# Kernel tuning notes

Hardware: AMD Instinct MI355X
Metric: run time of the kernel (lower is better)

The kernel has to match this reference:

```python
import jax, jax.numpy as jnp
import numpy as np

B, S, D, H = 2, 2048, 1024, 16
DK = D // H


def setup_inputs() -> dict:
    key = jax.random.key(0)
    ks = jax.random.split(key, 7)
    q = jax.random.normal(ks[0], (B, S, D), dtype=jnp.float32)
    k = jax.random.normal(ks[1], (B, S, D), dtype=jnp.float32)
    v = jax.random.normal(ks[2], (B, S, D), dtype=jnp.float32)
    # causal mask: mask==0 positions get -1e9 before softmax
    mask = jnp.tril(jnp.ones((S, S), dtype=jnp.int32))[None, None, :, :]
    scale = 0.02
    w_q = jax.random.normal(ks[3], (D, D), dtype=jnp.float32) * scale
    w_k = jax.random.normal(ks[4], (D, D), dtype=jnp.float32) * scale
    w_v = jax.random.normal(ks[5], (D, D), dtype=jnp.float32) * scale
    w_o = jax.random.normal(ks[6], (D, D), dtype=jnp.float32) * scale
    return {"q": q, "k": k, "v": v, "mask": mask,
            "w_q": w_q, "w_k": w_k, "w_v": w_v, "w_o": w_o}


def reference(q, k, v, mask, w_q, w_k, w_v, w_o):
    # nn.Linear(bias=False): x @ W.T
    query = q @ w_q.T  # [B,S,D]
    key = k @ w_k.T
    value = v @ w_v.T
    # split heads -> [B,H,S,DK]
    query = query.reshape(B, S, H, DK).transpose(0, 2, 1, 3)
    key = key.reshape(B, S, H, DK).transpose(0, 2, 1, 3)
    value = value.reshape(B, S, H, DK).transpose(0, 2, 1, 3)
    scores = jnp.einsum('bhqd,bhkd->bhqk', query, key) / jnp.sqrt(
        jnp.asarray(DK, dtype=query.dtype))
    scores = jnp.where(mask == 0, jnp.asarray(-1e9, scores.dtype), scores)
    attn = jax.nn.softmax(scores, axis=-1)  # dropout p=0.0 -> identity
    x = jnp.einsum('bhqk,bhkd->bhqd', attn, value)  # [B,H,S,DK]
    x = x.transpose(0, 2, 1, 3).reshape(B, S, D)
    return x @ w_o.T
```

## Files before the change

kernel.cpp:

```cpp
#include <hip/hip_runtime.h>

typedef __attribute__((ext_vector_type(8))) short short8;
typedef __attribute__((ext_vector_type(4))) float f32x4;

#define DEVI static __device__ __forceinline__

constexpr int BB = 2, SS = 2048, DD = 1024, HH = 16, DKK = 64;
constexpr size_t QN = (size_t)BB * SS * DD;
constexpr size_t WN = (size_t)DD * DD;

constexpr size_t OFF_WQ = 3 * QN;
constexpr size_t OFF_WO = OFF_WQ + 3 * WN;
constexpr size_t OFF_QM = OFF_WQ + 4 * WN;
constexpr size_t OFF_KM = OFF_QM + QN;
constexpr size_t OFF_VM = OFF_QM + 2 * QN;
constexpr size_t OFF_XC = OFF_QM + 3 * QN;

DEVI unsigned short f2bf(float f) {
  unsigned int u = __float_as_uint(f);
  u = (u + 0x7fffu + ((u >> 16) & 1u)) >> 16;
  return (unsigned short)u;
}

DEVI f32x4 fzero() { f32x4 z = {0.f, 0.f, 0.f, 0.f}; return z; }

DEVI void gld16(const void* g, void* l) {
  __builtin_amdgcn_global_load_lds((__attribute__((address_space(1))) void*)g,
                                   (__attribute__((address_space(3))) void*)l,
                                   16, 0, 0);
}

DEVI short8 mk8u(unsigned int a, unsigned int b, unsigned int c, unsigned int d) {
  union { short8 s; unsigned int u[4]; } x;
  x.u[0] = a; x.u[1] = b; x.u[2] = c; x.u[3] = d;
  return x.s;
}

DEVI short8 mk8q(unsigned long long lo, unsigned long long hi) {
  union { short8 s; unsigned long long q[2]; } x;
  x.q[0] = lo; x.q[1] = hi;
  return x.s;
}

DEVI unsigned int pkbf(float a, float b) {
  return __builtin_amdgcn_perm(__float_as_uint(b), __float_as_uint(a), 0x07060302u);
}

#define VMBAR(N) asm volatile("s_waitcnt vmcnt(" #N ")\n\ts_barrier" ::: "memory")
#define LGKM0                                      \
  do {                                             \
    asm volatile("s_waitcnt lgkmcnt(0)" ::: "memory"); \
    __builtin_amdgcn_sched_barrier(0);             \
  } while (0)

__global__ __launch_bounds__(256) void convert_all(
    const float* __restrict__ q, const float* __restrict__ k,
    const float* __restrict__ v, const float* __restrict__ wq,
    const float* __restrict__ wk, const float* __restrict__ wv,
    const float* __restrict__ wo, unsigned short* __restrict__ ws) {
  size_t t = (size_t)blockIdx.x * 256 + threadIdx.x;
  size_t e = t * 4;
  const float* src;
  size_t base, idx;
  if (e < 3 * QN) {
    size_t a = e >> 22;
    idx = e & (QN - 1);
    src = (a == 0) ? q : (a == 1) ? k : v;
    base = a * QN;
  } else {
    size_t r = e - 3 * QN;
    size_t a = r >> 20;
    idx = r & (WN - 1);
    src = (a == 0) ? wq : (a == 1) ? wk : (a == 2) ? wv : wo;
    base = 3 * QN + a * WN;
  }
  float4 f = *(const float4*)(src + idx);
  ushort4 o;
  o.x = f2bf(f.x); o.y = f2bf(f.y); o.z = f2bf(f.z); o.w = f2bf(f.w);
  *(ushort4*)(ws + base + idx) = o;
}

__global__ __launch_bounds__(512, 2) void proj_gemm(unsigned short* __restrict__ ws) {
  __shared__ unsigned short lds[65536];
  const int tid = threadIdx.x;
  const int w = tid >> 6, l = tid & 63;
  const int lr = l & 15, qd = l >> 4, l7 = l & 7, l3 = l >> 3;
  const int wr = w >> 2, wc = w & 3;

  const int orig = blockIdx.x;
  const int swz = (orig & 7) * 24 + (orig >> 3);
  const int mt = swz >> 2, nt = swz & 3;
  const int z = mt >> 4;
  const int m0 = (mt & 15) * 256, n0 = nt * 256;

  const unsigned short* Ab = ws + (size_t)z * QN;
  const unsigned short* Wb = ws + OFF_WQ + (size_t)z * WN;
  unsigned short* O = ws + OFF_QM + (size_t)z * QN;

  const bool vz = (z == 2);
  const unsigned short* src0 = vz ? Ab : Wb;
  const unsigned short* src1 = vz ? Wb : Ab;
  const int base0 = vz ? m0 : n0;
  const int base1 = vz ? n0 : m0;

  f32x4 acc[8][4];
#pragma unroll
  for (int i = 0; i < 8; ++i)
#pragma unroll
    for (int j = 0; j < 4; ++j) acc[i][j] = fzero();

  auto stage = [&](int buf, int ab, int h, int kt) {
    const unsigned short* src = ab ? src1 : src0;
    const int rc0 = (ab ? base1 : base0) + h * 128 + w * 8 + l3;
    const int kofs = kt * 64 + ((l7 ^ l3) * 8);
    unsigned short* d = &lds[buf * 32768 + ab * 16384 + h * 8192 + w * 512];
#pragma unroll
    for (int u = 0; u < 2; ++u)
      gld16(src + (size_t)(rc0 + u * 64) * DD + kofs, d + u * 4096);
  };
  auto rdA = [&](int buf, int fi, int ks) -> short8 {
    const int rg = (fi * 2 + wr) * 16 + lr;
    const int c2 = (ks * 4 + qd) ^ l7;
    return *(const short8*)&lds[buf * 32768 + rg * 64 + c2 * 8];
  };
  auto rdB = [&](int buf, int fj, int ks) -> short8 {
    const int rg = (fj * 4 + wc) * 16 + lr;
    const int c2 = (ks * 4 + qd) ^ l7;
    return *(const short8*)&lds[buf * 32768 + 16384 + rg * 64 + c2 * 8];
  };

  stage(0, 0, 0, 0);
  stage(0, 1, 0, 0);
  stage(0, 1, 1, 0);
  stage(0, 0, 1, 0);

  constexpr int NT = DD / 64;
#pragma unroll 1
  for (int t = 0; t < NT; ++t) {
    const int rb = t & 1, wb = rb ^ 1;
    const bool g = (t + 1 < NT);
    short8 af[4][2], bf[2][2], bh[2][2];

    VMBAR(4);
    if (g) stage(wb, 0, 0, t + 1);
#pragma unroll
    for (int mi = 0; mi < 4; ++mi)
#pragma unroll
      for (int ks = 0; ks < 2; ++ks) af[mi][ks] = rdA(rb, mi, ks);
#pragma unroll
    for (int nj = 0; nj < 2; ++nj)
#pragma unroll
      for (int ks = 0; ks < 2; ++ks) bf[nj][ks] = rdB(rb, nj, ks);
    LGKM0;
    __builtin_amdgcn_s_setprio(1);
#pragma unroll
    for (int mi = 0; mi < 4; ++mi)
#pragma unroll
      for (int nj = 0; nj < 2; ++nj)
#pragma unroll
        for (int ks = 0; ks < 2; ++ks)
          acc[mi][nj] = __builtin_amdgcn_mfma_f32_16x16x32_bf16(
              af[mi][ks], bf[nj][ks], acc[mi][nj], 0, 0, 0);
    __builtin_amdgcn_s_setprio(0);

    if (g) { VMBAR(4); } else { VMBAR(2); }
    if (g) stage(wb, 1, 0, t + 1);
#pragma unroll
    for (int nj = 0; nj < 2; ++nj)
#pragma unroll
      for (int ks = 0; ks < 2; ++ks) bh[nj][ks] = rdB(rb, 2 + nj, ks);
    LGKM0;
    __builtin_amdgcn_s_setprio(1);
#pragma unroll
    for (int mi = 0; mi < 4; ++mi)
#pragma unroll
      for (int nj = 0; nj < 2; ++nj)
#pragma unroll
        for (int ks = 0; ks < 2; ++ks)
          acc[mi][2 + nj] = __builtin_amdgcn_mfma_f32_16x16x32_bf16(
              af[mi][ks], bh[nj][ks], acc[mi][2 + nj], 0, 0, 0);
    __builtin_amdgcn_s_setprio(0);

    if (g) { VMBAR(4); } else { VMBAR(0); }
    if (g) stage(wb, 1, 1, t + 1);
#pragma unroll
    for (int mi = 0; mi < 4; ++mi)
#pragma unroll
      for (int ks = 0; ks < 2; ++ks) af[mi][ks] = rdA(rb, 4 + mi, ks);
    LGKM0;
    __builtin_amdgcn_s_setprio(1);
#pragma unroll
    for (int mi = 0; mi < 4; ++mi)
#pragma unroll
      for (int nj = 0; nj < 2; ++nj)
#pragma unroll
        for (int ks = 0; ks < 2; ++ks)
          acc[4 + mi][nj] = __builtin_amdgcn_mfma_f32_16x16x32_bf16(
              af[mi][ks], bf[nj][ks], acc[4 + mi][nj], 0, 0, 0);
    __builtin_amdgcn_s_setprio(0);

    if (g) stage(wb, 0, 1, t + 1);
    __builtin_amdgcn_s_setprio(1);
#pragma unroll
    for (int mi = 0; mi < 4; ++mi)
#pragma unroll
      for (int nj = 0; nj < 2; ++nj)
#pragma unroll
        for (int ks = 0; ks < 2; ++ks)
          acc[4 + mi][2 + nj] = __builtin_amdgcn_mfma_f32_16x16x32_bf16(
              af[mi][ks], bh[nj][ks], acc[4 + mi][2 + nj], 0, 0, 0);
    __builtin_amdgcn_s_setprio(0);
  }

  if (vz) {
#pragma unroll
    for (int fi = 0; fi < 8; ++fi)
#pragma unroll
      for (int fj = 0; fj < 4; ++fj) {
        const int n = n0 + (fj * 4 + wc) * 16 + lr;
        const int h = n >> 6, dk = n & 63;
        const int m = m0 + (fi * 2 + wr) * 16 + qd * 4;
        const int b = m >> 11, s = m & 2047;
        ushort4 pk;
        pk.x = f2bf(acc[fi][fj][0]); pk.y = f2bf(acc[fi][fj][1]);
        pk.z = f2bf(acc[fi][fj][2]); pk.w = f2bf(acc[fi][fj][3]);
        *(ushort4*)&O[((size_t)(b * HH + h) * DKK + dk) * SS + s] = pk;
      }
  } else {
#pragma unroll
    for (int fi = 0; fi < 8; ++fi)
#pragma unroll
      for (int fj = 0; fj < 4; ++fj) {
        const int nb = n0 + (fi * 2 + wr) * 16 + qd * 4;
        const int h = nb >> 6, dk = nb & 63;
        const int m = m0 + (fj * 4 + wc) * 16 + lr;
        const int b = m >> 11, s = m & 2047;
        ushort4 pk;
        pk.x = f2bf(acc[fi][fj][0]); pk.y = f2bf(acc[fi][fj][1]);
        pk.z = f2bf(acc[fi][fj][2]); pk.w = f2bf(acc[fi][fj][3]);
        *(ushort4*)&O[((size_t)(b * HH + h) * SS + s) * DKK + dk] = pk;
      }
  }
}

__global__ __launch_bounds__(512) void flash_attn(
    const unsigned short* __restrict__ Qm, const unsigned short* __restrict__ Km,
    const unsigned short* __restrict__ Vt, unsigned short* __restrict__ Xc) {
  __shared__ unsigned short Kl[2][4096];
  __shared__ unsigned short Vl[2][4096];
  const int head = blockIdx.x, py = blockIdx.y, b = blockIdx.z;
  const int p = b ? 15 - py : py;
  const int tid = threadIdx.x, w = tid >> 6, l = tid & 63, lr = l & 15, qd = l >> 4;
  const int slr = lr ^ ((lr >> 3) << 2);
  const size_t bh = (size_t)(b * HH + head);
  const unsigned short* Qb = Qm + bh * SS * DKK;
  const unsigned short* Kb = Km + bh * SS * DKK;
  const unsigned short* Vb = Vt + bh * DKK * SS;

  const bool heavy = (w < 4);
  const int qt = heavy ? (2 * p + 1) : (2 * p);
  const int nkv = 2 * p + 2;
  const int qrow = qt * 64 + (w & 3) * 16 + lr;

  const int s0 = heavy ? w : (w - 4);
  const int s1 = s0 + 4;
  const int loOff = ((qd >> 1) * 16 + slr) * 8 + (qd & 1) * 4;
  const int hiOff = ((2 + (qd >> 1)) * 16 + slr) * 8 + (qd & 1) * 4;

  short8 qf0 = *(const short8*)&Qb[(size_t)qrow * DKK + qd * 8];
  short8 qf1 = *(const short8*)&Qb[(size_t)qrow * DKK + 32 + qd * 8];

  f32x4 o[4];
#pragma unroll
  for (int i = 0; i < 4; ++i) o[i] = fzero();
  float ll = 0.f;
  const float c1 = 0.18033688011112042f;
  const float mc = 8.0f * c1;

  {
    if (heavy) {
      gld16(&Kb[(size_t)((s0 >> 1) * 16 + lr) * DKK + (s0 & 1) * 32 + qd * 8],
            &Kl[0][s0 * 512]);
      gld16(&Kb[(size_t)((s1 >> 1) * 16 + lr) * DKK + (s1 & 1) * 32 + qd * 8],
            &Kl[0][s1 * 512]);
    } else {
      gld16(&Vb[(size_t)((s0 >> 1) * 16 + slr) * SS + (s0 & 1) * 32 + qd * 8],
            &Vl[0][s0 * 512]);
      gld16(&Vb[(size_t)((s1 >> 1) * 16 + slr) * SS + (s1 & 1) * 32 + qd * 8],
            &Vl[0][s1 * 512]);
    }
  }

#pragma unroll 1
  for (int kv = 0; kv < nkv; ++kv) {
    __syncthreads();
    const int cur = kv & 1;
    if (kv + 1 < nkv) {
      const int kv0n = (kv + 1) * 64;
      if (heavy) {
        gld16(&Kb[(size_t)(kv0n + (s0 >> 1) * 16 + lr) * DKK + (s0 & 1) * 32 + qd * 8],
              &Kl[cur ^ 1][s0 * 512]);
        gld16(&Kb[(size_t)(kv0n + (s1 >> 1) * 16 + lr) * DKK + (s1 & 1) * 32 + qd * 8],
              &Kl[cur ^ 1][s1 * 512]);
      } else {
        gld16(&Vb[(size_t)((s0 >> 1) * 16 + slr) * SS + kv0n + (s0 & 1) * 32 + qd * 8],
              &Vl[cur ^ 1][s0 * 512]);
        gld16(&Vb[(size_t)((s1 >> 1) * 16 + slr) * SS + kv0n + (s1 & 1) * 32 + qd * 8],
              &Vl[cur ^ 1][s1 * 512]);
      }
    }

    if (kv <= qt) {
      const int kv0 = kv * 64;
      short8 kf0[4], kf1[4];
#pragma unroll
      for (int nt = 0; nt < 4; ++nt) {
        kf0[nt] = *(const short8*)&Kl[cur][(nt * 2 + 0) * 512 + l * 8];
        kf1[nt] = *(const short8*)&Kl[cur][(nt * 2 + 1) * 512 + l * 8];
      }
      f32x4 sc[4];
      __builtin_amdgcn_s_setprio(1);
#pragma unroll
      for (int nt = 0; nt < 4; ++nt) {
        f32x4 zz = fzero();
        zz = __builtin_amdgcn_mfma_f32_16x16x32_bf16(kf0[nt], qf0, zz, 0, 0, 0);
        sc[nt] = __builtin_amdgcn_mfma_f32_16x16x32_bf16(kf1[nt], qf1, zz, 0, 0, 0);
      }
      __builtin_amdgcn_s_setprio(0);
      if (kv == qt) {
#pragma unroll
        for (int nt = 0; nt < 4; ++nt)
#pragma unroll
          for (int i = 0; i < 4; ++i) {
            const int kvi = kv0 + nt * 16 + qd * 4 + i;
            if (kvi > qrow) sc[nt][i] = -3e38f;
          }
      }

#pragma unroll
      for (int nt = 0; nt < 4; ++nt)
#pragma unroll
        for (int i = 0; i < 4; ++i) {
          const float pp = exp2f(fmaf(sc[nt][i], c1, -mc));
          sc[nt][i] = pp;
          ll += pp;
        }

      unsigned int pd[4][2];
#pragma unroll
      for (int f = 0; f < 4; ++f) {
        pd[f][0] = pkbf(sc[f][0], sc[f][1]);
        pd[f][1] = pkbf(sc[f][2], sc[f][3]);
      }

#pragma unroll
      for (int kh = 0; kh < 2; ++kh) {
        short8 bfr = mk8u(pd[2 * kh][0], pd[2 * kh][1],
                          pd[2 * kh + 1][0], pd[2 * kh + 1][1]);
        unsigned long long vlo[4], vhi[4];
#pragma unroll
        for (int mt = 0; mt < 4; ++mt) {
          const int sbase = (mt * 2 + kh) * 512;
          vlo[mt] = *(const unsigned long long*)&Vl[cur][sbase + loOff];
          vhi[mt] = *(const unsigned long long*)&Vl[cur][sbase + hiOff];
        }
        __builtin_amdgcn_s_setprio(1);
#pragma unroll
        for (int mt = 0; mt < 4; ++mt)
          o[mt] = __builtin_amdgcn_mfma_f32_16x16x32_bf16(mk8q(vlo[mt], vhi[mt]),
                                                          bfr, o[mt], 0, 0, 0);
        __builtin_amdgcn_s_setprio(0);
      }
    }
  }

  ll += __shfl_xor(ll, 16);
  ll += __shfl_xor(ll, 32);

  const float inv = 1.0f / ll;
  unsigned short* Xr = Xc + ((size_t)b * SS + qrow) * DD + (size_t)head * DKK;
#pragma unroll
  for (int mt = 0; mt < 4; ++mt)
#pragma unroll
    for (int i = 0; i < 4; ++i)
      Xr[mt * 16 + qd * 4 + i] = f2bf(o[mt][i] * inv);
}

__global__ __launch_bounds__(256, 2) void out_gemm(
    const unsigned short* __restrict__ Xc, const unsigned short* __restrict__ Wo,
    float* __restrict__ out) {
  __shared__ unsigned short lds[32768];
  const int tid = threadIdx.x;
  const int w = tid >> 6, l = tid & 63;
  const int lr = l & 15, qd = l >> 4, l7 = l & 7, l3 = l >> 3;
  const int wr = w >> 1, wc = w & 1;
  const int m0 = blockIdx.x * 128, n0 = blockIdx.y * 128;

  f32x4 acc[4][4];
#pragma unroll
  for (int i = 0; i < 4; ++i)
#pragma unroll
    for (int j = 0; j < 4; ++j) acc[i][j] = fzero();

  auto stage = [&](int buf, int ab, int h, int kt) {
    const unsigned short* src = ab ? Wo : Xc;
    const int rc0 = (ab ? n0 : m0) + h * 64 + w * 8 + l3;
    const int kofs = kt * 64 + ((l7 ^ l3) * 8);
    unsigned short* d = &lds[buf * 16384 + ab * 8192 + h * 4096 + w * 512];
#pragma unroll
    for (int u = 0; u < 2; ++u)
      gld16(src + (size_t)(rc0 + u * 32) * DD + kofs, d + u * 2048);
  };
  auto rdA = [&](int buf, int mf, int ks) -> short8 {
    const int rg = mf * 16 + lr;
    const int c2 = (ks * 4 + qd) ^ l7;
    return *(const short8*)&lds[buf * 16384 + rg * 64 + c2 * 8];
  };
  auto rdB = [&](int buf, int nf, int ks) -> short8 {
    const int rg = nf * 16 + lr;
    const int c2 = (ks * 4 + qd) ^ l7;
    return *(const short8*)&lds[buf * 16384 + 8192 + rg * 64 + c2 * 8];
  };

  stage(0, 0, 0, 0);
  stage(0, 1, 0, 0);
  stage(0, 1, 1, 0);
  stage(0, 0, 1, 0);

  constexpr int NT = DD / 64;
#pragma unroll 1
  for (int t = 0; t < NT; ++t) {
    const int rb = t & 1, wb = rb ^ 1;
    const bool g = (t + 1 < NT);
    short8 af[2][2], bf[2][2], bh[2][2];

    VMBAR(4);
    if (g) stage(wb, 0, 0, t + 1);
#pragma unroll
    for (int mi = 0; mi < 2; ++mi)
#pragma unroll
      for (int ks = 0; ks < 2; ++ks) af[mi][ks] = rdA(rb, mi * 2 + wr, ks);
#pragma unroll
    for (int nj = 0; nj < 2; ++nj)
#pragma unroll
      for (int ks = 0; ks < 2; ++ks) bf[nj][ks] = rdB(rb, nj * 2 + wc, ks);
    LGKM0;
    __builtin_amdgcn_s_setprio(1);
#pragma unroll
    for (int mi = 0; mi < 2; ++mi)
#pragma unroll
      for (int nj = 0; nj < 2; ++nj)
#pragma unroll
        for (int ks = 0; ks < 2; ++ks)
          acc[mi][nj] = __builtin_amdgcn_mfma_f32_16x16x32_bf16(
              af[mi][ks], bf[nj][ks], acc[mi][nj], 0, 0, 0);
    __builtin_amdgcn_s_setprio(0);

    if (g) { VMBAR(4); } else { VMBAR(2); }
    if (g) stage(wb, 1, 0, t + 1);
#pragma unroll
    for (int nj = 0; nj < 2; ++nj)
#pragma unroll
      for (int ks = 0; ks < 2; ++ks) bh[nj][ks] = rdB(rb, (2 + nj) * 2 + wc, ks);
    LGKM0;
    __builtin_amdgcn_s_setprio(1);
#pragma unroll
    for (int mi = 0; mi < 2; ++mi)
#pragma unroll
      for (int nj = 0; nj < 2; ++nj)
#pragma unroll
        for (int ks = 0; ks < 2; ++ks)
          acc[mi][2 + nj] = __builtin_amdgcn_mfma_f32_16x16x32_bf16(
              af[mi][ks], bh[nj][ks], acc[mi][2 + nj], 0, 0, 0);
    __builtin_amdgcn_s_setprio(0);

    if (g) { VMBAR(4); } else { VMBAR(0); }
    if (g) stage(wb, 1, 1, t + 1);
#pragma unroll
    for (int mi = 0; mi < 2; ++mi)
#pragma unroll
      for (int ks = 0; ks < 2; ++ks) af[mi][ks] = rdA(rb, (2 + mi) * 2 + wr, ks);
    LGKM0;
    __builtin_amdgcn_s_setprio(1);
#pragma unroll
    for (int mi = 0; mi < 2; ++mi)
#pragma unroll
      for (int nj = 0; nj < 2; ++nj)
#pragma unroll
        for (int ks = 0; ks < 2; ++ks)
          acc[2 + mi][nj] = __builtin_amdgcn_mfma_f32_16x16x32_bf16(
              af[mi][ks], bf[nj][ks], acc[2 + mi][nj], 0, 0, 0);
    __builtin_amdgcn_s_setprio(0);

    if (g) stage(wb, 0, 1, t + 1);
    __builtin_amdgcn_s_setprio(1);
#pragma unroll
    for (int mi = 0; mi < 2; ++mi)
#pragma unroll
      for (int nj = 0; nj < 2; ++nj)
#pragma unroll
        for (int ks = 0; ks < 2; ++ks)
          acc[2 + mi][2 + nj] = __builtin_amdgcn_mfma_f32_16x16x32_bf16(
              af[mi][ks], bh[nj][ks], acc[2 + mi][2 + nj], 0, 0, 0);
    __builtin_amdgcn_s_setprio(0);
  }

#pragma unroll
  for (int a = 0; a < 4; ++a)
#pragma unroll
    for (int c = 0; c < 4; ++c) {
      const int n = n0 + (c * 2 + wc) * 16 + lr;
#pragma unroll
      for (int i = 0; i < 4; ++i) {
        const int m = m0 + (a * 2 + wr) * 16 + qd * 4 + i;
        out[(size_t)m * DD + n] = acc[a][c][i];
      }
    }
}

extern "C" void kernel_launch(void* const* d_in, const int* in_sizes, int n_in,
                              void* d_out, int out_size, void* d_ws, size_t ws_size,
                              hipStream_t stream) {
  (void)in_sizes; (void)n_in; (void)out_size; (void)ws_size;
  const float* q  = (const float*)d_in[0];
  const float* k  = (const float*)d_in[1];
  const float* v  = (const float*)d_in[2];
  const float* wq = (const float*)d_in[4];
  const float* wk = (const float*)d_in[5];
  const float* wv = (const float*)d_in[6];
  const float* wo = (const float*)d_in[7];
  unsigned short* ws = (unsigned short*)d_ws;
  float* out = (float*)d_out;

  convert_all<<<dim3(16384), dim3(256), 0, stream>>>(q, k, v, wq, wk, wv, wo, ws);
  proj_gemm<<<dim3(192), dim3(512), 0, stream>>>(ws);
  flash_attn<<<dim3(16, 16, 2), dim3(512), 0, stream>>>(ws + OFF_QM, ws + OFF_KM,
                                                        ws + OFF_VM, ws + OFF_XC);
  out_gemm<<<dim3(32, 8), dim3(256), 0, stream>>>(ws + OFF_XC, ws + OFF_WO, out);
}
```

Measured before the change: 216.6 us.

## Rebalance flash attention by pairing query tiles and splitting the heavy tile's KV range

Each block now pairs query tile p with tile 31-p. Warps 0-3 walk the first half of the heavy tile's KV range. Warps 4-7 first finish the light tile, then take the rest of the heavy tile's KV range using their own K/V buffers. The two partial results are merged through shared memory at the end. The goal is equal work per block and per warp group under the causal mask. The cost is four LDS buffers (64KB), loads issued per group, and an extra reduction step.

```diff
diff --git a/kernel.cpp b/kernel.cpp
--- a/kernel.cpp
+++ b/kernel.cpp
@@ -246,8 +246,12 @@
 __global__ __launch_bounds__(512) void flash_attn(
     const unsigned short* __restrict__ Qm, const unsigned short* __restrict__ Km,
     const unsigned short* __restrict__ Vt, unsigned short* __restrict__ Xc) {
-  __shared__ unsigned short Kl[2][4096];
-  __shared__ unsigned short Vl[2][4096];
+  __shared__ unsigned short sh[32768];
+  unsigned short* KA = sh;
+  unsigned short* VA = sh + 8192;
+  unsigned short* KL = sh + 16384;
+  unsigned short* VL = sh + 24576;
+
   const int head = blockIdx.x, py = blockIdx.y, b = blockIdx.z;
   const int p = b ? 15 - py : py;
   const int tid = threadIdx.x, w = tid >> 6, l = tid & 63, lr = l & 15, qd = l >> 4;
@@ -258,15 +262,13 @@
   const unsigned short* Vb = Vt + bh * DKK * SS;
 
   const bool heavy = (w < 4);
-  const int qt = heavy ? (2 * p + 1) : (2 * p);
-  const int nkv = 2 * p + 2;
-  const int qrow = qt * 64 + (w & 3) * 16 + lr;
-
-  const int s0 = heavy ? w : (w - 4);
-  const int s1 = s0 + 4;
+  const int g = w & 3;
+  const int At = 31 - p, Bt = p;
+  const int s0 = g, s1 = g + 4;
   const int loOff = ((qd >> 1) * 16 + slr) * 8 + (qd & 1) * 4;
   const int hiOff = ((2 + (qd >> 1)) * 16 + slr) * 8 + (qd & 1) * 4;
 
+  int qrow = (heavy ? At : Bt) * 64 + g * 16 + lr;
   short8 qf0 = *(const short8*)&Qb[(size_t)qrow * DKK + qd * 8];
   short8 qf1 = *(const short8*)&Qb[(size_t)qrow * DKK + 32 + qd * 8];
 
@@ -277,113 +279,157 @@
   const float c1 = 0.18033688011112042f;
   const float mc = 8.0f * c1;
 
-  {
+  auto stK = [&](unsigned short* dst, int buf, int kv) {
+    unsigned short* d = dst + buf * 4096;
+    gld16(&Kb[(size_t)(kv * 64 + (s0 >> 1) * 16 + lr) * DKK + (s0 & 1) * 32 + qd * 8],
+          d + s0 * 512);
+    gld16(&Kb[(size_t)(kv * 64 + (s1 >> 1) * 16 + lr) * DKK + (s1 & 1) * 32 + qd * 8],
+          d + s1 * 512);
+  };
+  auto stV = [&](unsigned short* dst, int buf, int kv) {
+    unsigned short* d = dst + buf * 4096;
+    gld16(&Vb[(size_t)((s0 >> 1) * 16 + slr) * SS + kv * 64 + (s0 & 1) * 32 + qd * 8],
+          d + s0 * 512);
+    gld16(&Vb[(size_t)((s1 >> 1) * 16 + slr) * SS + kv * 64 + (s1 & 1) * 32 + qd * 8],
+          d + s1 * 512);
+  };
+
+  auto body = [&](const unsigned short* Kc, const unsigned short* Vc,
+                  int kv, int myqt) {
+    const int kv0 = kv * 64;
+    short8 kf0[4], kf1[4];
+#pragma unroll
+    for (int nt = 0; nt < 4; ++nt) {
+      kf0[nt] = *(const short8*)&Kc[(nt * 2 + 0) * 512 + l * 8];
+      kf1[nt] = *(const short8*)&Kc[(nt * 2 + 1) * 512 + l * 8];
+    }
+    f32x4 sc[4];
+    __builtin_amdgcn_s_setprio(1);
+#pragma unroll
+    for (int nt = 0; nt < 4; ++nt) {
+      f32x4 zz = fzero();
+      zz = __builtin_amdgcn_mfma_f32_16x16x32_bf16(kf0[nt], qf0, zz, 0, 0, 0);
+      sc[nt] = __builtin_amdgcn_mfma_f32_16x16x32_bf16(kf1[nt], qf1, zz, 0, 0, 0);
+    }
+    __builtin_amdgcn_s_setprio(0);
+    if (kv == myqt) {
+#pragma unroll
+      for (int nt = 0; nt < 4; ++nt)
+#pragma unroll
+        for (int i = 0; i < 4; ++i) {
+          const int kvi = kv0 + nt * 16 + qd * 4 + i;
+          if (kvi > qrow) sc[nt][i] = -3e38f;
+        }
+    }
+#pragma unroll
+    for (int nt = 0; nt < 4; ++nt)
+#pragma unroll
+      for (int i = 0; i < 4; ++i) {
+        const float pp = exp2f(fmaf(sc[nt][i], c1, -mc));
+        sc[nt][i] = pp;
+        ll += pp;
+      }
+    unsigned int pd[4][2];
+#pragma unroll
+    for (int f = 0; f < 4; ++f) {
+      pd[f][0] = pkbf(sc[f][0], sc[f][1]);
+      pd[f][1] = pkbf(sc[f][2], sc[f][3]);
+    }
+#pragma unroll
+    for (int kh = 0; kh < 2; ++kh) {
+      short8 bfr = mk8u(pd[2 * kh][0], pd[2 * kh][1],
+                        pd[2 * kh + 1][0], pd[2 * kh + 1][1]);
+      unsigned long long vlo[4], vhi[4];
+#pragma unroll
+      for (int mt = 0; mt < 4; ++mt) {
+        const int sbase = (mt * 2 + kh) * 512;
+        vlo[mt] = *(const unsigned long long*)&Vc[sbase + loOff];
+        vhi[mt] = *(const unsigned long long*)&Vc[sbase + hiOff];
+      }
+      __builtin_amdgcn_s_setprio(1);
+#pragma unroll
+      for (int mt = 0; mt < 4; ++mt)
+        o[mt] = __builtin_amdgcn_mfma_f32_16x16x32_bf16(mk8q(vlo[mt], vhi[mt]),
+                                                        bfr, o[mt], 0, 0, 0);
+      __builtin_amdgcn_s_setprio(0);
+    }
+  };
+
+  if (heavy) { stK(KA, 0, 0); stV(VA, 0, 0); }
+
+#pragma unroll 1
+  for (int t = 0; t <= 16; ++t) {
+    __syncthreads();
+    const int cura = t & 1;
     if (heavy) {
-      gld16(&Kb[(size_t)((s0 >> 1) * 16 + lr) * DKK + (s0 & 1) * 32 + qd * 8],
-            &Kl[0][s0 * 512]);
-      gld16(&Kb[(size_t)((s1 >> 1) * 16 + lr) * DKK + (s1 & 1) * 32 + qd * 8],
-            &Kl[0][s1 * 512]);
+      if (t < 16) { stK(KA, cura ^ 1, t + 1); stV(VA, cura ^ 1, t + 1); }
+      body(KA + cura * 4096, VA + cura * 4096, t, At);
     } else {
-      gld16(&Vb[(size_t)((s0 >> 1) * 16 + slr) * SS + (s0 & 1) * 32 + qd * 8],
-            &Vl[0][s0 * 512]);
-      gld16(&Vb[(size_t)((s1 >> 1) * 16 + slr) * SS + (s1 & 1) * 32 + qd * 8],
-            &Vl[0][s1 * 512]);
-    }
-  }
-
-#pragma unroll 1
-  for (int kv = 0; kv < nkv; ++kv) {
-    __syncthreads();
-    const int cur = kv & 1;
-    if (kv + 1 < nkv) {
-      const int kv0n = (kv + 1) * 64;
-      if (heavy) {
-        gld16(&Kb[(size_t)(kv0n + (s0 >> 1) * 16 + lr) * DKK + (s0 & 1) * 32 + qd * 8],
-              &Kl[cur ^ 1][s0 * 512]);
-        gld16(&Kb[(size_t)(kv0n + (s1 >> 1) * 16 + lr) * DKK + (s1 & 1) * 32 + qd * 8],
-              &Kl[cur ^ 1][s1 * 512]);
-      } else {
-        gld16(&Vb[(size_t)((s0 >> 1) * 16 + slr) * SS + kv0n + (s0 & 1) * 32 + qd * 8],
-              &Vl[cur ^ 1][s0 * 512]);
-        gld16(&Vb[(size_t)((s1 >> 1) * 16 + slr) * SS + kv0n + (s1 & 1) * 32 + qd * 8],
-              &Vl[cur ^ 1][s1 * 512]);
-      }
-    }
-
-    if (kv <= qt) {
-      const int kv0 = kv * 64;
-      short8 kf0[4], kf1[4];
-#pragma unroll
-      for (int nt = 0; nt < 4; ++nt) {
-        kf0[nt] = *(const short8*)&Kl[cur][(nt * 2 + 0) * 512 + l * 8];
-        kf1[nt] = *(const short8*)&Kl[cur][(nt * 2 + 1) * 512 + l * 8];
-      }
-      f32x4 sc[4];
-      __builtin_amdgcn_s_setprio(1);
-#pragma unroll
-      for (int nt = 0; nt < 4; ++nt) {
-        f32x4 zz = fzero();
-        zz = __builtin_amdgcn_mfma_f32_16x16x32_bf16(kf0[nt], qf0, zz, 0, 0, 0);
-        sc[nt] = __builtin_amdgcn_mfma_f32_16x16x32_bf16(kf1[nt], qf1, zz, 0, 0, 0);
-      }
-      __builtin_amdgcn_s_setprio(0);
-      if (kv == qt) {
-#pragma unroll
-        for (int nt = 0; nt < 4; ++nt)
-#pragma unroll
-          for (int i = 0; i < 4; ++i) {
-            const int kvi = kv0 + nt * 16 + qd * 4 + i;
-            if (kvi > qrow) sc[nt][i] = -3e38f;
-          }
-      }
-
-#pragma unroll
-      for (int nt = 0; nt < 4; ++nt)
-#pragma unroll
-        for (int i = 0; i < 4; ++i) {
-          const float pp = exp2f(fmaf(sc[nt][i], c1, -mc));
-          sc[nt][i] = pp;
-          ll += pp;
+      if (t >= p && t + 1 <= 15) {
+        const int kvn = t + 17 - p;
+        const int bufn = (t - p) & 1;
+        stK(KL, bufn, kvn);
+        stV(VL, bufn, kvn);
+      }
+      if (t <= 15) {
+        const bool ph1 = (t <= p);
+        const int kv = ph1 ? t : t + 16 - p;
+        const int myqt = ph1 ? Bt : At;
+        const unsigned short* Kc =
+            ph1 ? (KA + cura * 4096) : (KL + ((t - p - 1) & 1) * 4096);
+        const unsigned short* Vc =
+            ph1 ? (VA + cura * 4096) : (VL + ((t - p - 1) & 1) * 4096);
+        body(Kc, Vc, kv, myqt);
+        if (t == p) {
+          float llB = ll;
+          llB += __shfl_xor(llB, 16);
+          llB += __shfl_xor(llB, 32);
+          const float invB = 1.0f / llB;
+          unsigned short* Xr =
+              Xc + ((size_t)b * SS + qrow) * DD + (size_t)head * DKK;
+#pragma unroll
+          for (int mt = 0; mt < 4; ++mt)
+#pragma unroll
+            for (int i = 0; i < 4; ++i)
+              Xr[mt * 16 + qd * 4 + i] = f2bf(o[mt][i] * invB);
+#pragma unroll
+          for (int i = 0; i < 4; ++i) o[i] = fzero();
+          ll = 0.f;
+          qrow = At * 64 + g * 16 + lr;
+          qf0 = *(const short8*)&Qb[(size_t)qrow * DKK + qd * 8];
+          qf1 = *(const short8*)&Qb[(size_t)qrow * DKK + 32 + qd * 8];
         }
-
-      unsigned int pd[4][2];
-#pragma unroll
-      for (int f = 0; f < 4; ++f) {
-        pd[f][0] = pkbf(sc[f][0], sc[f][1]);
-        pd[f][1] = pkbf(sc[f][2], sc[f][3]);
-      }
-
-#pragma unroll
-      for (int kh = 0; kh < 2; ++kh) {
-        short8 bfr = mk8u(pd[2 * kh][0], pd[2 * kh][1],
-                          pd[2 * kh + 1][0], pd[2 * kh + 1][1]);
-        unsigned long long vlo[4], vhi[4];
-#pragma unroll
-        for (int mt = 0; mt < 4; ++mt) {
-          const int sbase = (mt * 2 + kh) * 512;
-          vlo[mt] = *(const unsigned long long*)&Vl[cur][sbase + loOff];
-          vhi[mt] = *(const unsigned long long*)&Vl[cur][sbase + hiOff];
-        }
-        __builtin_amdgcn_s_setprio(1);
-#pragma unroll
-        for (int mt = 0; mt < 4; ++mt)
-          o[mt] = __builtin_amdgcn_mfma_f32_16x16x32_bf16(mk8q(vlo[mt], vhi[mt]),
-                                                          bfr, o[mt], 0, 0, 0);
-        __builtin_amdgcn_s_setprio(0);
-      }
-    }
-  }
-
-  ll += __shfl_xor(ll, 16);
-  ll += __shfl_xor(ll, 32);
-
-  const float inv = 1.0f / ll;
-  unsigned short* Xr = Xc + ((size_t)b * SS + qrow) * DD + (size_t)head * DKK;
-#pragma unroll
-  for (int mt = 0; mt < 4; ++mt)
-#pragma unroll
-    for (int i = 0; i < 4; ++i)
-      Xr[mt * 16 + qd * 4 + i] = f2bf(o[mt][i] * inv);
+      }
+    }
+  }
+
+  __syncthreads();
+  float* shp = (float*)sh;
+  const int pbase = (g * 64 + l) * 17;
+  if (!heavy) {
+#pragma unroll
+    for (int mt = 0; mt < 4; ++mt)
+#pragma unroll
+      for (int i = 0; i < 4; ++i) shp[pbase + mt * 4 + i] = o[mt][i];
+    shp[pbase + 16] = ll;
+  }
+  __syncthreads();
+  if (heavy) {
+#pragma unroll
+    for (int mt = 0; mt < 4; ++mt)
+#pragma unroll
+      for (int i = 0; i < 4; ++i) o[mt][i] += shp[pbase + mt * 4 + i];
+    ll += shp[pbase + 16];
+    ll += __shfl_xor(ll, 16);
+    ll += __shfl_xor(ll, 32);
+    const float inv = 1.0f / ll;
+    unsigned short* Xr = Xc + ((size_t)b * SS + qrow) * DD + (size_t)head * DKK;
+#pragma unroll
+    for (int mt = 0; mt < 4; ++mt)
+#pragma unroll
+      for (int i = 0; i < 4; ++i)
+        Xr[mt * 16 + qd * 4 + i] = f2bf(o[mt][i] * inv);
+  }
 }
 
 __global__ __launch_bounds__(256, 2) void out_gemm(
```

Result: no change. 218.7 us (+1.0%).
